# Kernel optimization log

Measured on AMD Instinct MI355X. Metric: run time of the kernel, lower is better.

The kernel has to match this reference:

```python
import jax, jax.numpy as jnp
import numpy as np


def binarize(x):
    # sign to +/-1 (>=0 -> 1); forward value only (STE handled in bwd module)
    return jnp.where(x >= 0, 1.0, -1.0).astype(x.dtype)


def setup_inputs() -> dict:
    key = jax.random.key(0)
    k1, k2, k3 = jax.random.split(key, 3)
    B, D_IN, D_H, D_OUT = 16384, 4096, 4096, 1
    x = jax.random.normal(k1, (B, D_IN), dtype=jnp.float32)
    W1 = jax.random.normal(k2, (D_H, D_IN), dtype=jnp.float32) * 0.02
    W2 = jax.random.normal(k3, (D_OUT, D_H), dtype=jnp.float32) * 0.02
    return {"x": x, "W1": W1, "W2": W2}


def reference(x, W1, W2):
    # fc1: BinaryLinear (binarized weight, no bias) + BinaryTanh (hardtanh then sign)
    h = x @ binarize(W1).T                      # [B, D_H]
    h = binarize(jnp.clip(h, -1.0, 1.0))        # hardtanh + binarize -> +/-1
    # fc2: BinaryLinear + Sigmoid
    out = jax.nn.sigmoid(h @ binarize(W2).T)    # [B, 1]
    y_hat = jnp.squeeze((out >= 0.5).astype(jnp.float32))  # [B]
    return out, y_hat
```

## Files before the change

### kernel.cpp

```cpp
#include <hip/hip_runtime.h>
#include <stdint.h>


typedef int v4i  __attribute__((ext_vector_type(4)));
typedef int v16i __attribute__((ext_vector_type(16)));

#define B_ROWS   16384
#define DIM      4096
#define MT       64
#define NT       128
#define KT       64

#define WS_LOGIT  0
#define WS_W2S    65536
#define WS_B      69632
#define WS_A      (69632 + 16777216)
#define WS_NEEDED ((size_t)WS_A + 268435456ULL)

__device__ __forceinline__ void dma16(const void* g, void* l) {
    __builtin_amdgcn_global_load_lds(
        (const __attribute__((address_space(1))) void*)g,
        (__attribute__((address_space(3))) void*)l, 16, 0, 0);
}

__global__ void pack_x_frag_kernel(const float* __restrict__ x, int8_t* __restrict__ wsA) {
    __shared__ __align__(16) int8_t tile[16384];
    const int mb32 = blockIdx.x, t = threadIdx.x;
    const int r = t >> 3;
    const int c = t & 7;
    const int kh = (c >> 2) & 1;
    const int L = kh * 32 + r;
    const int ldsQ = L * 16 + (c & 3) * 4;
    const float* srcRow = x + ((size_t)(mb32 * 32 + r) << 12);
    int8_t* dstBase = wsA + ((size_t)mb32 << 19);

    for (int kw = 0; kw < 32; ++kw) {
#pragma unroll
        for (int i = 0; i < 4; ++i) {
            const int j = c + 8 * i;
            float4 f = ((const float4*)(srcRow + (kw << 7)))[j];
            float fv[4] = {f.x, f.y, f.z, f.w};
            int dig[4][4];
#pragma unroll
            for (int e = 0; e < 4; ++e) {
                int v = __float2int_rn(fv[e] * 67108864.0f);
#pragma unroll
                for (int d = 0; d < 4; ++d) {
                    int b = (int)(int8_t)(v & 0xff);
                    dig[e][d] = b & 0xff;
                    v = (v - b) >> 8;
                }
            }
#pragma unroll
            for (int d = 0; d < 4; ++d) {
                uint32_t wrd = (uint32_t)dig[0][d] | ((uint32_t)dig[1][d] << 8)
                             | ((uint32_t)dig[2][d] << 16) | ((uint32_t)dig[3][d] << 24);
                *(uint32_t*)(tile + i * 4096 + d * 1024 + ldsQ) = wrd;
            }
        }
        __syncthreads();
        {
            const int4* s = (const int4*)tile;
            int4* dst = (int4*)(dstBase + ((size_t)kw << 14));
#pragma unroll
            for (int q = 0; q < 4; ++q) dst[t + 256 * q] = s[t + 256 * q];
        }
        __syncthreads();
    }
}

__global__ void pack_x_kernel(float* __restrict__ x) {
    const int b = blockIdx.x, t = threadIdx.x;
    float* row = x + (size_t)b * DIM;
    float f[16];
#pragma unroll
    for (int i = 0; i < 4; ++i) {
        float4 v = ((const float4*)(row + t * 16))[i];
        f[i*4+0] = v.x; f[i*4+1] = v.y; f[i*4+2] = v.z; f[i*4+3] = v.w;
    }
    __syncthreads();
    uint32_t wds[4][4];
#pragma unroll
    for (int j = 0; j < 4; ++j) {
#pragma unroll
        for (int d = 0; d < 4; ++d) wds[d][j] = 0u;
#pragma unroll
        for (int i = 0; i < 4; ++i) {
            int v = __float2int_rn(f[j*4+i] * 67108864.0f);
#pragma unroll
            for (int d = 0; d < 4; ++d) {
                int bb = (int)(int8_t)(v & 0xff);
                wds[d][j] |= (uint32_t)(bb & 0xff) << (8 * i);
                v = (v - bb) >> 8;
            }
        }
    }
    int8_t* rowb = (int8_t*)row;
#pragma unroll
    for (int d = 0; d < 4; ++d) {
        int4 o; o.x = (int)wds[d][0]; o.y = (int)wds[d][1];
        o.z = (int)wds[d][2]; o.w = (int)wds[d][3];
        *(int4*)(rowb + d * DIM + t * 16) = o;
    }
}

__global__ void pack_w1_kernel(const float* __restrict__ W1, int8_t* __restrict__ wsB) {
    const int tg = blockIdx.x * 256 + threadIdx.x;
    const int n  = tg >> 8;
    const int k0 = (tg & 255) << 4;
    const float* src = W1 + (size_t)n * DIM + k0;
    uint32_t w[4];
#pragma unroll
    for (int j = 0; j < 4; ++j) {
        float4 v = ((const float4*)src)[j];
        uint32_t b0 = (v.x >= 0.f) ? 0x01u : 0xFFu;
        uint32_t b1 = (v.y >= 0.f) ? 0x01u : 0xFFu;
        uint32_t b2 = (v.z >= 0.f) ? 0x01u : 0xFFu;
        uint32_t b3 = (v.w >= 0.f) ? 0x01u : 0xFFu;
        w[j] = b0 | (b1 << 8) | (b2 << 16) | (b3 << 24);
    }
    const int nb = n >> 7, kt = k0 >> 6;
    const int nsub = (n >> 5) & 3, ks = (k0 >> 5) & 1;
    const int L = (n & 31) | (((k0 >> 4) & 1) << 5);
    const size_t off = ((size_t)(nb * 64 + kt) << 13) + (nsub << 11) + (ks << 10) + (L << 4);
    int4 o; o.x = (int)w[0]; o.y = (int)w[1]; o.z = (int)w[2]; o.w = (int)w[3];
    *(int4*)(wsB + off) = o;
}

__global__ void pack_w2_kernel(const float* __restrict__ W2, int8_t* __restrict__ w2s) {
    const int j = blockIdx.x * 256 + threadIdx.x;
    if (j < DIM) w2s[j] = (W2[j] >= 0.f) ? (int8_t)1 : (int8_t)-1;
}

#define LOAD_AF(dst, kt_) do {                                             \
    const int8_t* _p = aBase + ((size_t)(kt_) << 13);                      \
    _Pragma("unroll") for (int _s = 0; _s < 2; ++_s)                       \
    _Pragma("unroll") for (int _d = 0; _d < 4; ++_d)                       \
        dst[_s * 4 + _d] = *(const v4i*)(_p + (_s << 12) + (_d << 10));    \
} while (0)

#define DMA_B(kt_, buf_) do {                                              \
    const int8_t* _s = bSrcL + ((size_t)(kt_) << 13);                      \
    int8_t* _dst = &bT[(buf_)][w << 11];                                   \
    dma16(_s, _dst); dma16(_s + 1024, _dst + 1024);                        \
} while (0)

#define MFMA_STEP(af_, buf_) do {                                          \
    const int8_t* _bc = &bT[(buf_)][(wx << 12) + (lane << 4)];             \
    v4i _bf[2][2];                                                         \
    _Pragma("unroll") for (int _s = 0; _s < 2; ++_s)                       \
    _Pragma("unroll") for (int _n = 0; _n < 2; ++_n)                       \
        _bf[_s][_n] = *(const v4i*)(_bc + (_n << 11) + (_s << 10));        \
    _Pragma("unroll") for (int _s = 0; _s < 2; ++_s)                       \
    _Pragma("unroll") for (int _n = 0; _n < 2; ++_n)                       \
    _Pragma("unroll") for (int _d = 0; _d < 4; ++_d)                       \
        acc[_n][_d] = __builtin_amdgcn_mfma_i32_32x32x32_i8(               \
            af_[_s * 4 + _d], _bf[_s][_n], acc[_n][_d], 0, 0, 0);          \
} while (0)

__launch_bounds__(256, 2)
__global__ void gemm_direct_kernel(const int8_t* __restrict__ wsA,
                                   const int8_t* __restrict__ wsB,
                                   const int8_t* __restrict__ w2s,
                                   int* __restrict__ logit) {
    __shared__ __align__(16) int8_t bT[2][8192];

    const int bid = blockIdx.x;
    const int nb = bid & 31, mb = bid >> 5;
    const int t = threadIdx.x, lane = t & 63, w = t >> 6;
    const int wy = w >> 1, wx = w & 1;

    v16i acc[2][4];
#pragma unroll
    for (int n = 0; n < 2; ++n)
#pragma unroll
        for (int d = 0; d < 4; ++d)
#pragma unroll
            for (int i = 0; i < 16; ++i) acc[n][d][i] = 0;

    const int8_t* aBase = wsA + ((size_t)(mb * 2 + wy) << 19) + (lane << 4);
    const int8_t* bSrcL = wsB + ((size_t)(nb * 64) << 13) + (w << 11) + (lane << 4);

    v4i afA[8], afB[8];
    DMA_B(0, 0);
    LOAD_AF(afA, 0);

    for (int kt2 = 0; kt2 < 32; ++kt2) {
        const int kt = kt2 * 2;
        __syncthreads();
        if (kt < 63) { DMA_B(kt + 1, 1); LOAD_AF(afB, kt + 1); }
        MFMA_STEP(afA, 0);
        __syncthreads();
        if (kt2 < 31) { DMA_B(kt + 2, 0); LOAD_AF(afA, kt + 2); }
        MFMA_STEP(afB, 1);
    }

    const int half = lane >> 5, col = lane & 31;
    int psum[16];
#pragma unroll
    for (int r = 0; r < 16; ++r) psum[r] = 0;
#pragma unroll
    for (int n = 0; n < 2; ++n) {
        const int j = nb * NT + wx * 64 + n * 32 + col;
        const int w2v = (int)w2s[j];
#pragma unroll
        for (int r = 0; r < 16; ++r) {
            long long h = (long long)acc[n][0][r]
                        + ((long long)acc[n][1][r] << 8)
                        + ((long long)acc[n][2][r] << 16)
                        + ((long long)acc[n][3][r] << 24);
            psum[r] += (h >= 0) ? w2v : -w2v;
        }
    }
#pragma unroll
    for (int r = 0; r < 16; ++r) {
#pragma unroll
        for (int m = 1; m <= 16; m <<= 1)
            psum[r] += __shfl_xor(psum[r], m, 64);
    }
    if (col == 0) {
        const int rowBase = mb * MT + wy * 32 + 4 * half;
#pragma unroll
        for (int r = 0; r < 16; ++r)
            atomicAdd(logit + rowBase + (r & 3) + 8 * (r >> 2), psum[r]);
    }
}

__launch_bounds__(256, 2)
__global__ void gemm_kernel(const int8_t* __restrict__ xq,
                            const int8_t* __restrict__ wsB,
                            const int8_t* __restrict__ w2s,
                            int* __restrict__ logit) {
    __shared__ __align__(16) int8_t aT[4 * MT * KT];
    __shared__ __align__(16) int8_t bT[NT * KT];

    const int bid = blockIdx.x;
    const int nb = bid & 31, mb = bid >> 5;
    const int t = threadIdx.x, lane = t & 63, w = t >> 6;
    const int wy = w >> 1, wx = w & 1;

    v16i acc[2][4];
#pragma unroll
    for (int n = 0; n < 2; ++n)
#pragma unroll
        for (int d = 0; d < 4; ++d)
#pragma unroll
            for (int i = 0; i < 16; ++i) acc[n][d][i] = 0;

    const int8_t* aSrc = xq + (size_t)(mb * MT + lane) * (4 * DIM) + w * DIM;
    const int8_t* bSrc = wsB + ((size_t)(nb * 64) << 13) + t * 32;
    const int aDst = w * (MT * KT) + ((lane >> 5) << 11) + ((lane & 31) << 4);

    for (int kt = 0; kt < DIM / KT; ++kt) {
#pragma unroll
        for (int k16 = 0; k16 < 4; ++k16) {
            v4i v = *(const v4i*)(aSrc + kt * KT + k16 * 16);
            *(v4i*)(aT + aDst + ((k16 >> 1) << 10) + ((k16 & 1) << 9)) = v;
        }
        {
            const v4i* s = (const v4i*)(bSrc + ((size_t)kt << 13));
            *(v4i*)(bT + t * 32)      = s[0];
            *(v4i*)(bT + t * 32 + 16) = s[1];
        }
        __syncthreads();
#pragma unroll
        for (int s = 0; s < 2; ++s) {
            v4i af[4], bf[2];
#pragma unroll
            for (int d = 0; d < 4; ++d)
                af[d] = *(const v4i*)(aT + d * (MT * KT) + (wy << 11) + (s << 10) + (lane << 4));
#pragma unroll
            for (int n = 0; n < 2; ++n)
                bf[n] = *(const v4i*)(bT + ((wx * 2 + n) << 11) + (s << 10) + (lane << 4));
#pragma unroll
            for (int n = 0; n < 2; ++n)
#pragma unroll
                for (int d = 0; d < 4; ++d)
                    acc[n][d] = __builtin_amdgcn_mfma_i32_32x32x32_i8(af[d], bf[n], acc[n][d], 0, 0, 0);
        }
        __syncthreads();
    }

    const int half = lane >> 5, col = lane & 31;
    int psum[16];
#pragma unroll
    for (int r = 0; r < 16; ++r) psum[r] = 0;
#pragma unroll
    for (int n = 0; n < 2; ++n) {
        const int j = nb * NT + wx * 64 + n * 32 + col;
        const int w2v = (int)w2s[j];
#pragma unroll
        for (int r = 0; r < 16; ++r) {
            long long h = (long long)acc[n][0][r]
                        + ((long long)acc[n][1][r] << 8)
                        + ((long long)acc[n][2][r] << 16)
                        + ((long long)acc[n][3][r] << 24);
            psum[r] += (h >= 0) ? w2v : -w2v;
        }
    }
#pragma unroll
    for (int r = 0; r < 16; ++r) {
#pragma unroll
        for (int m = 1; m <= 16; m <<= 1)
            psum[r] += __shfl_xor(psum[r], m, 64);
    }
    if (col == 0) {
        const int rowBase = mb * MT + wy * 32 + 4 * half;
#pragma unroll
        for (int r = 0; r < 16; ++r)
            atomicAdd(logit + rowBase + (r & 3) + 8 * (r >> 2), psum[r]);
    }
}

__global__ void finalize_kernel(const int* __restrict__ logit, float* __restrict__ out) {
    const int b = blockIdx.x * 256 + threadIdx.x;
    if (b < B_ROWS) {
        const int l = logit[b];
        out[b]          = 1.f / (1.f + expf(-(float)l));
        out[B_ROWS + b] = (l >= 0) ? 1.f : 0.f;
    }
}

extern "C" void kernel_launch(void* const* d_in, const int* in_sizes, int n_in,
                              void* d_out, int out_size, void* d_ws, size_t ws_size,
                              hipStream_t stream) {
    float*       x   = (float*)d_in[0];
    const float* W1  = (const float*)d_in[1];
    const float* W2  = (const float*)d_in[2];
    float*       out = (float*)d_out;

    int8_t* ws    = (int8_t*)d_ws;
    int*    logit = (int*)(ws + WS_LOGIT);
    int8_t* w2s   = ws + WS_W2S;
    int8_t* wsB   = ws + WS_B;

    hipMemsetAsync(logit, 0, B_ROWS * sizeof(int), stream);
    pack_w1_kernel<<<DIM, 256, 0, stream>>>(W1, wsB);
    pack_w2_kernel<<<16, 256, 0, stream>>>(W2, w2s);

    if (ws_size >= WS_NEEDED) {
        int8_t* wsA = ws + WS_A;
        pack_x_frag_kernel<<<B_ROWS / 32, 256, 0, stream>>>(x, wsA);
        gemm_direct_kernel<<<(B_ROWS / MT) * (DIM / NT), 256, 0, stream>>>(wsA, wsB, w2s, logit);
    } else {
        pack_x_kernel<<<B_ROWS, 256, 0, stream>>>(x);
        gemm_kernel<<<(B_ROWS / MT) * (DIM / NT), 256, 0, stream>>>((const int8_t*)x, wsB, w2s, logit);
    }
    finalize_kernel<<<B_ROWS / 256, 256, 0, stream>>>(logit, out);
}
```

Before: 1.665 ms.

## Stage four K-tiles of B per LDS buffer to cut barrier count

The GEMM main loop now DMAs four K-tiles of the packed binary weight matrix into LDS per stage (32 KB per buffer, 64 KB double-buffered) instead of one. This cuts __syncthreads from 64 to 16 per block while keeping the per-tile A-register double buffering. The larger LDS footprint may limit occupancy, since two blocks per CU now need 128 KB of LDS, and each stage issues a larger burst of DMA.

```diff
diff --git a/kernel.cpp b/kernel.cpp
--- a/kernel.cpp
+++ b/kernel.cpp
@@ -139,14 +139,15 @@
         dst[_s * 4 + _d] = *(const v4i*)(_p + (_s << 12) + (_d << 10));    \
 } while (0)
 
-#define DMA_B(kt_, buf_) do {                                              \
-    const int8_t* _s = bSrcL + ((size_t)(kt_) << 13);                      \
-    int8_t* _dst = &bT[(buf_)][w << 11];                                   \
-    dma16(_s, _dst); dma16(_s + 1024, _dst + 1024);                        \
+#define DMA_BG(g_, b_) do {                                                \
+    const int8_t* _s = bSrcW + ((size_t)(g_) << 15);                       \
+    int8_t* _d = &bT[(b_)][w << 13];                                       \
+    _Pragma("unroll") for (int _c = 0; _c < 8; ++_c)                       \
+        dma16(_s + _c * 1024, _d + _c * 1024);                             \
 } while (0)
 
-#define MFMA_STEP(af_, buf_) do {                                          \
-    const int8_t* _bc = &bT[(buf_)][(wx << 12) + (lane << 4)];             \
+#define MFMA_STEP(af_, buf_, ktl_) do {                                    \
+    const int8_t* _bc = &bT[(buf_)][((ktl_) << 13) + (wx << 12) + (lane << 4)]; \
     v4i _bf[2][2];                                                         \
     _Pragma("unroll") for (int _s = 0; _s < 2; ++_s)                       \
     _Pragma("unroll") for (int _n = 0; _n < 2; ++_n)                       \
@@ -163,7 +164,7 @@
                                    const int8_t* __restrict__ wsB,
                                    const int8_t* __restrict__ w2s,
                                    int* __restrict__ logit) {
-    __shared__ __align__(16) int8_t bT[2][8192];
+    __shared__ __align__(16) int8_t bT[2][32768];
 
     const int bid = blockIdx.x;
     const int nb = bid & 31, mb = bid >> 5;
@@ -179,20 +180,24 @@
             for (int i = 0; i < 16; ++i) acc[n][d][i] = 0;
 
     const int8_t* aBase = wsA + ((size_t)(mb * 2 + wy) << 19) + (lane << 4);
-    const int8_t* bSrcL = wsB + ((size_t)(nb * 64) << 13) + (w << 11) + (lane << 4);
-
-    v4i afA[8], afB[8];
-    DMA_B(0, 0);
-    LOAD_AF(afA, 0);
-
-    for (int kt2 = 0; kt2 < 32; ++kt2) {
-        const int kt = kt2 * 2;
-        __syncthreads();
-        if (kt < 63) { DMA_B(kt + 1, 1); LOAD_AF(afB, kt + 1); }
-        MFMA_STEP(afA, 0);
-        __syncthreads();
-        if (kt2 < 31) { DMA_B(kt + 2, 0); LOAD_AF(afA, kt + 2); }
-        MFMA_STEP(afB, 1);
+    const int8_t* bSrcW = wsB + ((size_t)(nb * 64) << 13) + (w << 13) + (lane << 4);
+
+    v4i af0[8], af1[8];
+    DMA_BG(0, 0);
+    LOAD_AF(af0, 0);
+
+    for (int g = 0; g < 16; ++g) {
+        const int b = g & 1;
+        __syncthreads();
+        LOAD_AF(af1, 4 * g + 1);
+        if (g < 15) DMA_BG(g + 1, b ^ 1);
+        MFMA_STEP(af0, b, 0);
+        LOAD_AF(af0, 4 * g + 2);
+        MFMA_STEP(af1, b, 1);
+        LOAD_AF(af1, 4 * g + 3);
+        MFMA_STEP(af0, b, 2);
+        if (g < 15) LOAD_AF(af0, 4 * g + 4);
+        MFMA_STEP(af1, b, 3);
     }
 
     const int half = lane >> 5, col = lane & 31;
```

After: 1.828 ms. +9.8%, slower.
